# Performance work log

Hardware: AMD Instinct MI355X
Metric: run time of the kernel (lower is better)

The kernel has to match this reference:

```python
import jax, jax.numpy as jnp
import numpy as np

N, K, D, R = 846, 64, 256, 75   # n_drug, neighbor_sample_size, embedding_num, n_relation
BN_EPS = 1e-5


def setup_inputs() -> dict:
    key = jax.random.key(0)
    ks = jax.random.split(key, 12)
    return {
        "drug_name": jnp.arange(N, dtype=jnp.int32),
        "adj_tail": jax.random.randint(ks[0], (N, K), 0, N, dtype=jnp.int32),
        "adj_relation": jax.random.randint(ks[1], (N, K), 0, R, dtype=jnp.int32),
        "drug_table": jax.random.normal(ks[2], (N, D), jnp.float32),
        "rela_table": jax.random.normal(ks[3], (R, D), jnp.float32),
        "ent_table": jax.random.normal(ks[4], (N, D), jnp.float32),
        "W1": jax.random.normal(ks[5], (N, D, D), jnp.float32),
        "b1": jax.random.normal(ks[6], (K, D), jnp.float32),
        "W2": jax.random.normal(ks[7], (N, D, D), jnp.float32),
        "b2": jax.random.normal(ks[8], (K, D), jnp.float32),
        "lin_w": jax.random.normal(ks[9], (2 * D, D), jnp.float32) * (1.0 / np.sqrt(2 * D)),
        "lin_b": jnp.zeros((D,), jnp.float32),
        "bn_w": jnp.ones((D,), jnp.float32),
        "bn_b": jnp.zeros((D,), jnp.float32),
    }


def reference(drug_name, adj_tail, adj_relation, drug_table, rela_table, ent_table,
              W1, b1, W2, b2, lin_w, lin_b, bn_w, bn_b):
    drug_emb = drug_table[drug_name]            # [N, D]
    rela_emb = rela_table[adj_relation]         # [N, K, D]
    ent_emb = ent_table[adj_tail]               # [N, K, D]

    # broadcast multiply then two per-node batched GEMMs with bias + relu
    drug_rel = drug_emb[:, None, :] * rela_emb  # [N, K, D]
    h = jax.nn.relu(jnp.einsum('nkd,nde->nke', drug_rel, W1) + b1)
    h = jnp.einsum('nkd,nde->nke', h, W2) + b2  # [N, K, D]

    # score per neighbor, softmax over neighbors, weighted aggregation
    score = jax.nn.softmax(h.sum(axis=-1), axis=1)        # [N, K]
    weighted = jnp.einsum('nk,nkd->nd', score, ent_emb)   # [N, D]

    drug_e = jnp.concatenate([weighted, drug_emb], axis=1)  # [N, 2D]
    x = jax.nn.relu(drug_e @ lin_w + lin_b)                  # [N, D]

    # BatchNorm1d in training mode (biased variance), weight/bias init 1/0
    mean = x.mean(axis=0)
    var = x.var(axis=0)
    return (x - mean) / jnp.sqrt(var + BN_EPS) * bn_w + bn_b
```

## Files before the change

### kernel.cpp

```cpp
#include <hip/hip_runtime.h>
#include <math.h>

#define NN 846
#define KK 64
#define DD 256
constexpr float BN_EPS = 1e-5f;

__device__ __forceinline__ float wave_reduce_sum(float v) {
#pragma unroll
  for (int m = 32; m > 0; m >>= 1) v += __shfl_xor(v, m, 64);
  return v;
}

__device__ __forceinline__ void stage8(const float* gsrc, float* ldst, int wv, int lane) {
#pragma unroll
  for (int r = 0; r < 2; ++r) {
    const int row = 2 * wv + r;
    __builtin_amdgcn_global_load_lds(
        (const __attribute__((address_space(1))) void*)(gsrc + row * DD + lane * 4),
        (__attribute__((address_space(3))) void*)(ldst + row * DD),
        16, 0, 0);
  }
}

extern "C" __global__ __launch_bounds__(256) void fused_gnn(
    const int* __restrict__ drug_name,
    const int* __restrict__ adj_tail,
    const int* __restrict__ adj_rel,
    const float* __restrict__ drug_table,
    const float* __restrict__ rela_table,
    const float* __restrict__ ent_table,
    const float* __restrict__ W1,
    const float* __restrict__ b1,
    const float* __restrict__ W2,
    const float* __restrict__ b2,
    const float* __restrict__ lin_w,
    const float* __restrict__ lin_b,
    float* __restrict__ x_out) {
  __shared__ float s_dr[64][68];
  __shared__ float s_w1[2][8][256];
  __shared__ float s_w2s[256];
  __shared__ float s_drug[256];
  __shared__ float s_de[512];
  __shared__ float s_b2s[64];
  __shared__ float s_score[64];
  __shared__ float s_logits[64];
  __shared__ int s_rel[64];
  __shared__ int s_tail[64];

  const int n = blockIdx.x;
  const int tid = threadIdx.x;
  const int lane = tid & 63;
  const int wv = tid >> 6;
  const int kr = tid >> 5;
  const int ec = tid & 31;
  const int e0 = ec * 8;
  const int k0 = kr * 8;

  if (tid < 64) {
    s_rel[tid] = adj_rel[n * KK + tid];
    s_tail[tid] = adj_tail[n * KK + tid];
  }
  const int dn = drug_name[n];
  s_drug[tid] = drug_table[(size_t)dn * DD + tid];

  const float* W1n = W1 + (size_t)n * DD * DD;
  const float* W2n = W2 + (size_t)n * DD * DD;

#pragma unroll 4
  for (int i = 0; i < 16; ++i) {
    const int k = wv * 16 + i;
    const float4 v = *(const float4*)(b2 + (size_t)k * DD + lane * 4);
    const float p = wave_reduce_sum(v.x + v.y + v.z + v.w);
    if (lane == 0) s_b2s[k] = p;
  }

  for (int i0 = 0; i0 < 64; i0 += 8) {
    float ps[8];
#pragma unroll
    for (int u = 0; u < 8; ++u) {
      const int r = wv * 64 + i0 + u;
      const float4 v = *(const float4*)(W2n + (size_t)r * DD + lane * 4);
      ps[u] = v.x + v.y + v.z + v.w;
    }
#pragma unroll
    for (int u = 0; u < 8; ++u) {
      const float p = wave_reduce_sum(ps[u]);
      if (lane == 0) s_w2s[wv * 64 + i0 + u] = p;
    }
  }

  float acc[8][8];
#pragma unroll
  for (int i = 0; i < 8; ++i)
#pragma unroll
    for (int j = 0; j < 8; ++j) acc[i][j] = 0.f;

  for (int c = 0; c < 4; ++c) {
    const int d0 = c * 64;
    __syncthreads();

    stage8(W1n + (size_t)d0 * DD, &s_w1[0][0][0], wv, lane);

    const float dv = s_drug[d0 + lane];
#pragma unroll 4
    for (int i = 0; i < 16; ++i) {
      const int k = wv * 16 + i;
      const float rl = rela_table[(size_t)s_rel[k] * DD + d0 + lane];
      s_dr[k][lane] = dv * rl;
    }
    __syncthreads();

    for (int s = 0; s < 8; ++s) {
      if (s) __syncthreads();
      if (s < 7) stage8(W1n + (size_t)(d0 + (s + 1) * 8) * DD, &s_w1[(s + 1) & 1][0][0], wv, lane);
      const int buf = s & 1;
#pragma unroll
      for (int dd4 = 0; dd4 < 8; dd4 += 4) {
        float4 a[8];
#pragma unroll
        for (int i = 0; i < 8; ++i) a[i] = *(const float4*)&s_dr[k0 + i][s * 8 + dd4];
#pragma unroll
        for (int r = 0; r < 4; ++r) {
          const float4 w0 = *(const float4*)&s_w1[buf][dd4 + r][e0];
          const float4 w1v = *(const float4*)&s_w1[buf][dd4 + r][e0 + 4];
#pragma unroll
          for (int i = 0; i < 8; ++i) {
            const float av = (r == 0) ? a[i].x : (r == 1) ? a[i].y : (r == 2) ? a[i].z : a[i].w;
            acc[i][0] = fmaf(av, w0.x, acc[i][0]);
            acc[i][1] = fmaf(av, w0.y, acc[i][1]);
            acc[i][2] = fmaf(av, w0.z, acc[i][2]);
            acc[i][3] = fmaf(av, w0.w, acc[i][3]);
            acc[i][4] = fmaf(av, w1v.x, acc[i][4]);
            acc[i][5] = fmaf(av, w1v.y, acc[i][5]);
            acc[i][6] = fmaf(av, w1v.z, acc[i][6]);
            acc[i][7] = fmaf(av, w1v.w, acc[i][7]);
          }
        }
      }
    }
  }

  float lg[8];
#pragma unroll
  for (int i = 0; i < 8; ++i) {
    float partial = 0.f;
#pragma unroll
    for (int jj = 0; jj < 8; jj += 4) {
      const float4 bv = *(const float4*)(b1 + (size_t)(k0 + i) * DD + e0 + jj);
      const float4 wv2 = *(const float4*)&s_w2s[e0 + jj];
      partial = fmaf(fmaxf(acc[i][jj + 0] + bv.x, 0.f), wv2.x, partial);
      partial = fmaf(fmaxf(acc[i][jj + 1] + bv.y, 0.f), wv2.y, partial);
      partial = fmaf(fmaxf(acc[i][jj + 2] + bv.z, 0.f), wv2.z, partial);
      partial = fmaf(fmaxf(acc[i][jj + 3] + bv.w, 0.f), wv2.w, partial);
    }
#pragma unroll
    for (int m = 16; m > 0; m >>= 1) partial += __shfl_xor(partial, m, 64);
    lg[i] = partial;
  }
  if (ec == 0) {
#pragma unroll
    for (int i = 0; i < 8; ++i) s_logits[k0 + i] = lg[i] + s_b2s[k0 + i];
  }
  __syncthreads();

  if (wv == 0) {
    const float v = s_logits[lane];
    float mx = v;
#pragma unroll
    for (int m = 32; m > 0; m >>= 1) mx = fmaxf(mx, __shfl_xor(mx, m, 64));
    const float e = expf(v - mx);
    float ssum = e;
#pragma unroll
    for (int m = 32; m > 0; m >>= 1) ssum += __shfl_xor(ssum, m, 64);
    s_score[lane] = e / ssum;
  }
  __syncthreads();

  float wsum = 0.f;
  for (int k = 0; k < KK; ++k) {
    const float sc = s_score[k];
    if (sc > 1e-12f) wsum = fmaf(sc, ent_table[(size_t)s_tail[k] * DD + tid], wsum);
  }
  s_de[tid] = wsum;
  s_de[DD + tid] = s_drug[tid];
  __syncthreads();

  float xj = lin_b[tid];
#pragma unroll 8
  for (int i = 0; i < 2 * DD; ++i) xj = fmaf(s_de[i], lin_w[(size_t)i * DD + tid], xj);
  x_out[(size_t)n * DD + tid] = fmaxf(xj, 0.f);
}

extern "C" __global__ __launch_bounds__(256) void bn_kernel(
    const float* __restrict__ x,
    const float* __restrict__ bn_w,
    const float* __restrict__ bn_b,
    float* __restrict__ out) {
  __shared__ float s_s[4], s_s2[4];
  const int d = blockIdx.x;
  const int tid = threadIdx.x;
  const int lane = tid & 63, wv = tid >> 6;
  float v[4];
  float s = 0.f, s2 = 0.f;
#pragma unroll
  for (int u = 0; u < 4; ++u) {
    const int r = tid + u * 256;
    v[u] = (r < NN) ? x[(size_t)r * DD + d] : 0.f;
    s += v[u];
    s2 = fmaf(v[u], v[u], s2);
  }
  s = wave_reduce_sum(s);
  s2 = wave_reduce_sum(s2);
  if (lane == 0) { s_s[wv] = s; s_s2[wv] = s2; }
  __syncthreads();
  const float S = s_s[0] + s_s[1] + s_s[2] + s_s[3];
  const float S2 = s_s2[0] + s_s2[1] + s_s2[2] + s_s2[3];
  const float mean = S / (float)NN;
  const float var = S2 / (float)NN - mean * mean;
  const float scale = (1.0f / sqrtf(var + BN_EPS)) * bn_w[d];
  const float shift = bn_b[d];
#pragma unroll
  for (int u = 0; u < 4; ++u) {
    const int r = tid + u * 256;
    if (r < NN) out[(size_t)r * DD + d] = (v[u] - mean) * scale + shift;
  }
}

extern "C" void kernel_launch(void* const* d_in, const int* in_sizes, int n_in,
                              void* d_out, int out_size, void* d_ws, size_t ws_size,
                              hipStream_t stream) {
  const int* drug_name = (const int*)d_in[0];
  const int* adj_tail = (const int*)d_in[1];
  const int* adj_rel = (const int*)d_in[2];
  const float* drug_table = (const float*)d_in[3];
  const float* rela_table = (const float*)d_in[4];
  const float* ent_table = (const float*)d_in[5];
  const float* W1 = (const float*)d_in[6];
  const float* b1 = (const float*)d_in[7];
  const float* W2 = (const float*)d_in[8];
  const float* b2 = (const float*)d_in[9];
  const float* lin_w = (const float*)d_in[10];
  const float* lin_b = (const float*)d_in[11];
  const float* bn_w = (const float*)d_in[12];
  const float* bn_b = (const float*)d_in[13];

  float* x = (float*)d_ws;

  fused_gnn<<<NN, 256, 0, stream>>>(drug_name, adj_tail, adj_rel, drug_table,
                                    rela_table, ent_table, W1, b1, W2, b2,
                                    lin_w, lin_b, x);
  bn_kernel<<<DD, 256, 0, stream>>>(x, bn_w, bn_b, (float*)d_out);
}
```

Before: 582.6 us.

## Stream W1 from global into registers and fuse W2 row-sum into chunk loop

Drops the LDS double-buffered staging of W1 via global_load_lds and the per-stage barriers, so each thread reads its W1 slice straight from global memory inside the d-loop. The drug*relation tile is stored transposed so each thread gets its k-values with two float4 LDS reads. The W2 row-sum and b2 row-sum now use per-thread serial float4 sums instead of wave shuffles, with the W2 sum interleaved into the chunk loop. Launch bounds request 4 blocks per CU. The cost is redundant global loads of W1, since the 8 k-row groups each reread the same W1 data, and latency is no longer hidden by async staging.

```diff
diff --git a/kernel.cpp b/kernel.cpp
--- a/kernel.cpp
+++ b/kernel.cpp
@@ -12,18 +12,7 @@
   return v;
 }
 
-__device__ __forceinline__ void stage8(const float* gsrc, float* ldst, int wv, int lane) {
-#pragma unroll
-  for (int r = 0; r < 2; ++r) {
-    const int row = 2 * wv + r;
-    __builtin_amdgcn_global_load_lds(
-        (const __attribute__((address_space(1))) void*)(gsrc + row * DD + lane * 4),
-        (__attribute__((address_space(3))) void*)(ldst + row * DD),
-        16, 0, 0);
-  }
-}
-
-extern "C" __global__ __launch_bounds__(256) void fused_gnn(
+extern "C" __global__ __launch_bounds__(256, 4) void fused_gnn(
     const int* __restrict__ drug_name,
     const int* __restrict__ adj_tail,
     const int* __restrict__ adj_rel,
@@ -37,12 +26,11 @@
     const float* __restrict__ lin_w,
     const float* __restrict__ lin_b,
     float* __restrict__ x_out) {
-  __shared__ float s_dr[64][68];
-  __shared__ float s_w1[2][8][256];
+  __shared__ float s_dr_t[64][68];
   __shared__ float s_w2s[256];
+  __shared__ float s_b2p[64][5];
   __shared__ float s_drug[256];
   __shared__ float s_de[512];
-  __shared__ float s_b2s[64];
   __shared__ float s_score[64];
   __shared__ float s_logits[64];
   __shared__ int s_rel[64];
@@ -50,7 +38,6 @@
 
   const int n = blockIdx.x;
   const int tid = threadIdx.x;
-  const int lane = tid & 63;
   const int wv = tid >> 6;
   const int kr = tid >> 5;
   const int ec = tid & 31;
@@ -64,107 +51,117 @@
   const int dn = drug_name[n];
   s_drug[tid] = drug_table[(size_t)dn * DD + tid];
 
+  {
+    const int row = tid >> 2, seg = tid & 3;
+    const float4* p = (const float4*)(b2 + (size_t)row * DD + seg * 64);
+    float4 s4 = make_float4(0.f, 0.f, 0.f, 0.f);
+#pragma unroll
+    for (int j = 0; j < 16; ++j) {
+      const float4 v = p[j];
+      s4.x += v.x; s4.y += v.y; s4.z += v.z; s4.w += v.w;
+    }
+    s_b2p[row][seg] = s4.x + s4.y + s4.z + s4.w;
+  }
+
   const float* W1n = W1 + (size_t)n * DD * DD;
   const float* W2n = W2 + (size_t)n * DD * DD;
 
-#pragma unroll 4
-  for (int i = 0; i < 16; ++i) {
-    const int k = wv * 16 + i;
-    const float4 v = *(const float4*)(b2 + (size_t)k * DD + lane * 4);
-    const float p = wave_reduce_sum(v.x + v.y + v.z + v.w);
-    if (lane == 0) s_b2s[k] = p;
-  }
-
-  for (int i0 = 0; i0 < 64; i0 += 8) {
-    float ps[8];
-#pragma unroll
-    for (int u = 0; u < 8; ++u) {
-      const int r = wv * 64 + i0 + u;
-      const float4 v = *(const float4*)(W2n + (size_t)r * DD + lane * 4);
-      ps[u] = v.x + v.y + v.z + v.w;
-    }
-#pragma unroll
-    for (int u = 0; u < 8; ++u) {
-      const float p = wave_reduce_sum(ps[u]);
-      if (lane == 0) s_w2s[wv * 64 + i0 + u] = p;
-    }
-  }
-
   float acc[8][8];
 #pragma unroll
   for (int i = 0; i < 8; ++i)
 #pragma unroll
     for (int j = 0; j < 8; ++j) acc[i][j] = 0.f;
+
+  float w2acc = 0.f;
 
   for (int c = 0; c < 4; ++c) {
     const int d0 = c * 64;
     __syncthreads();
 
-    stage8(W1n + (size_t)d0 * DD, &s_w1[0][0][0], wv, lane);
-
-    const float dv = s_drug[d0 + lane];
-#pragma unroll 4
-    for (int i = 0; i < 16; ++i) {
-      const int k = wv * 16 + i;
-      const float rl = rela_table[(size_t)s_rel[k] * DD + d0 + lane];
-      s_dr[k][lane] = dv * rl;
-    }
+    {
+      const int kq = tid & 63;
+      const int dq = wv * 16;
+      const float* rr = rela_table + (size_t)s_rel[kq] * DD + d0 + dq;
+      const float4 r0 = *(const float4*)(rr + 0);
+      const float4 r1 = *(const float4*)(rr + 4);
+      const float4 r2 = *(const float4*)(rr + 8);
+      const float4 r3 = *(const float4*)(rr + 12);
+      const float rv[16] = {r0.x, r0.y, r0.z, r0.w, r1.x, r1.y, r1.z, r1.w,
+                            r2.x, r2.y, r2.z, r2.w, r3.x, r3.y, r3.z, r3.w};
+#pragma unroll
+      for (int u = 0; u < 16; ++u)
+        s_dr_t[dq + u][kq] = s_drug[d0 + dq + u] * rv[u];
+    }
+
+    {
+      const float4* p = (const float4*)(W2n + (size_t)tid * DD + d0);
+      float4 s4 = make_float4(0.f, 0.f, 0.f, 0.f);
+#pragma unroll
+      for (int j = 0; j < 16; ++j) {
+        const float4 v = p[j];
+        s4.x += v.x; s4.y += v.y; s4.z += v.z; s4.w += v.w;
+      }
+      w2acc += s4.x + s4.y + s4.z + s4.w;
+    }
+
     __syncthreads();
 
-    for (int s = 0; s < 8; ++s) {
-      if (s) __syncthreads();
-      if (s < 7) stage8(W1n + (size_t)(d0 + (s + 1) * 8) * DD, &s_w1[(s + 1) & 1][0][0], wv, lane);
-      const int buf = s & 1;
-#pragma unroll
-      for (int dd4 = 0; dd4 < 8; dd4 += 4) {
-        float4 a[8];
-#pragma unroll
-        for (int i = 0; i < 8; ++i) a[i] = *(const float4*)&s_dr[k0 + i][s * 8 + dd4];
-#pragma unroll
-        for (int r = 0; r < 4; ++r) {
-          const float4 w0 = *(const float4*)&s_w1[buf][dd4 + r][e0];
-          const float4 w1v = *(const float4*)&s_w1[buf][dd4 + r][e0 + 4];
-#pragma unroll
-          for (int i = 0; i < 8; ++i) {
-            const float av = (r == 0) ? a[i].x : (r == 1) ? a[i].y : (r == 2) ? a[i].z : a[i].w;
-            acc[i][0] = fmaf(av, w0.x, acc[i][0]);
-            acc[i][1] = fmaf(av, w0.y, acc[i][1]);
-            acc[i][2] = fmaf(av, w0.z, acc[i][2]);
-            acc[i][3] = fmaf(av, w0.w, acc[i][3]);
-            acc[i][4] = fmaf(av, w1v.x, acc[i][4]);
-            acc[i][5] = fmaf(av, w1v.y, acc[i][5]);
-            acc[i][6] = fmaf(av, w1v.z, acc[i][6]);
-            acc[i][7] = fmaf(av, w1v.w, acc[i][7]);
-          }
-        }
+    const float* wbase = W1n + (size_t)d0 * DD + e0;
+#pragma unroll 2
+    for (int dd = 0; dd < 64; ++dd) {
+      const float4 a0 = *(const float4*)&s_dr_t[dd][k0];
+      const float4 a1 = *(const float4*)&s_dr_t[dd][k0 + 4];
+      const float4 w0 = *(const float4*)(wbase + (size_t)dd * DD);
+      const float4 w1v = *(const float4*)(wbase + (size_t)dd * DD + 4);
+      const float av[8] = {a0.x, a0.y, a0.z, a0.w, a1.x, a1.y, a1.z, a1.w};
+#pragma unroll
+      for (int i = 0; i < 8; ++i) {
+        acc[i][0] = fmaf(av[i], w0.x, acc[i][0]);
+        acc[i][1] = fmaf(av[i], w0.y, acc[i][1]);
+        acc[i][2] = fmaf(av[i], w0.z, acc[i][2]);
+        acc[i][3] = fmaf(av[i], w0.w, acc[i][3]);
+        acc[i][4] = fmaf(av[i], w1v.x, acc[i][4]);
+        acc[i][5] = fmaf(av[i], w1v.y, acc[i][5]);
+        acc[i][6] = fmaf(av[i], w1v.z, acc[i][6]);
+        acc[i][7] = fmaf(av[i], w1v.w, acc[i][7]);
       }
     }
   }
 
+  s_w2s[tid] = w2acc;
+  __syncthreads();
+
+  const float4 wa = *(const float4*)&s_w2s[e0];
+  const float4 wb = *(const float4*)&s_w2s[e0 + 4];
   float lg[8];
 #pragma unroll
   for (int i = 0; i < 8; ++i) {
-    float partial = 0.f;
-#pragma unroll
-    for (int jj = 0; jj < 8; jj += 4) {
-      const float4 bv = *(const float4*)(b1 + (size_t)(k0 + i) * DD + e0 + jj);
-      const float4 wv2 = *(const float4*)&s_w2s[e0 + jj];
-      partial = fmaf(fmaxf(acc[i][jj + 0] + bv.x, 0.f), wv2.x, partial);
-      partial = fmaf(fmaxf(acc[i][jj + 1] + bv.y, 0.f), wv2.y, partial);
-      partial = fmaf(fmaxf(acc[i][jj + 2] + bv.z, 0.f), wv2.z, partial);
-      partial = fmaf(fmaxf(acc[i][jj + 3] + bv.w, 0.f), wv2.w, partial);
-    }
-#pragma unroll
-    for (int m = 16; m > 0; m >>= 1) partial += __shfl_xor(partial, m, 64);
-    lg[i] = partial;
+    const float* b1r = b1 + (size_t)(k0 + i) * DD + e0;
+    const float4 ba = *(const float4*)(b1r);
+    const float4 bb = *(const float4*)(b1r + 4);
+    float p = 0.f;
+    p = fmaf(fmaxf(acc[i][0] + ba.x, 0.f), wa.x, p);
+    p = fmaf(fmaxf(acc[i][1] + ba.y, 0.f), wa.y, p);
+    p = fmaf(fmaxf(acc[i][2] + ba.z, 0.f), wa.z, p);
+    p = fmaf(fmaxf(acc[i][3] + ba.w, 0.f), wa.w, p);
+    p = fmaf(fmaxf(acc[i][4] + bb.x, 0.f), wb.x, p);
+    p = fmaf(fmaxf(acc[i][5] + bb.y, 0.f), wb.y, p);
+    p = fmaf(fmaxf(acc[i][6] + bb.z, 0.f), wb.z, p);
+    p = fmaf(fmaxf(acc[i][7] + bb.w, 0.f), wb.w, p);
+#pragma unroll
+    for (int m = 16; m > 0; m >>= 1) p += __shfl_xor(p, m, 64);
+    lg[i] = p;
   }
   if (ec == 0) {
 #pragma unroll
-    for (int i = 0; i < 8; ++i) s_logits[k0 + i] = lg[i] + s_b2s[k0 + i];
+    for (int i = 0; i < 8; ++i)
+      s_logits[k0 + i] = lg[i] + s_b2p[k0 + i][0] + s_b2p[k0 + i][1] +
+                         s_b2p[k0 + i][2] + s_b2p[k0 + i][3];
   }
   __syncthreads();
 
   if (wv == 0) {
+    const int lane = tid & 63;
     const float v = s_logits[lane];
     float mx = v;
 #pragma unroll
```

New measurement: 651.1 us. +11.7%, slower.
